# Performance work log

Measured on AMD Instinct MI355X. Metric: run time of the kernel, lower is better.

## Reference

```python
import jax, jax.numpy as jnp
import numpy as np

DEPTH = 4  # truncation depth of the signature


def setup_inputs() -> dict:
    key = jax.random.key(0)
    # (N, L, C) batch of paths
    path = jax.random.normal(key, (32, 256, 8), dtype=jnp.float32)
    return {"path": path}


def _signature(path, depth):
    """Truncated path signature via Chen's relation over linear segments.

    For a linear segment with increment dx, its signature is exp(dx) in the
    tensor algebra: level j = dx^{\otimes j} / j!.  The signature of the
    concatenated path is the tensor-algebra product of segment signatures,
    computed with a scan over segments.
    """
    N, L, C = path.shape
    dx = path[:, 1:, :] - path[:, :-1, :]  # (N, L-1, C) increments

    def exp_levels(d):
        # levels of exp(d): e_j = d^{\otimes j} / j!, flattened to (N, C^j)
        levels = [d]
        for j in range(2, depth + 1):
            nxt = jnp.einsum('na,nb->nab', levels[-1], d).reshape(N, -1) / j
            levels.append(nxt)
        return levels

    def step(carry, d):
        # carry: tuple of (N, C^k) for k = 1..depth (levels of running signature)
        # Chen: new_k = sum_{i+j=k} carry_i (x) e_j, with carry_0 = e_0 = 1
        e = exp_levels(d)
        new = []
        for k in range(1, depth + 1):
            acc = carry[k - 1] + e[k - 1]  # i=k,j=0 and i=0,j=k terms
            for i in range(1, k):
                acc = acc + jnp.einsum(
                    'na,nb->nab', carry[i - 1], e[k - i - 1]
                ).reshape(N, -1)
            new.append(acc)
        return tuple(new), None

    init = tuple(jnp.zeros((N, C ** k), path.dtype) for k in range(1, depth + 1))
    final, _ = jax.lax.scan(step, init, jnp.swapaxes(dx, 0, 1))  # scan over L-1
    return jnp.concatenate(final, axis=-1)  # (N, C + C^2 + ... + C^depth)


def reference(path):
    return _signature(path, DEPTH)
```

## Files before the change

kernel.cpp:

```cpp
#include <hip/hip_runtime.h>

#define NBATCH 32
#define LPATH 256
#define NSEG 255
#define SIGLEN 4680
#define INV6 (1.0f/6.0f)
#define INV24 (1.0f/24.0f)

struct __align__(16) CBuf {
    float T4t[64 * 64];
    float T3b[8 * 68];
    float T2[64];
    float T1[8];
};

__global__ __launch_bounds__(512) void sig_kernel(const float* __restrict__ path,
                                                  float* __restrict__ out) {
    const int n = blockIdx.x;
    const int t = threadIdx.x;
    const int w = t >> 6;
    const int l = t & 63;
    const int a = l >> 3;
    const int b = l & 7;

    __shared__ float dbuf[NSEG * 8];
    __shared__ CBuf bufs[4];

    const float* prow = path + n * (LPATH * 8);
    for (int i = t; i < NSEG * 8; i += 512) dbuf[i] = prow[i + 8] - prow[i];
    __syncthreads();

    float S4[64];
    float S3[8];
    #pragma unroll
    for (int j = 0; j < 64; ++j) S4[j] = 0.f;
    #pragma unroll
    for (int c = 0; c < 8; ++c) S3[c] = 0.f;
    float S2 = 0.f, a1a = 0.f;

    const int s0 = w * 32;
    const int s1 = (s0 + 32 < NSEG) ? (s0 + 32) : NSEG;
    for (int s = s0; s < s1; ++s) {
        const float4 dlo = *(const float4*)&dbuf[s * 8];
        const float4 dhi = *(const float4*)&dbuf[s * 8 + 4];
        const float dr[8] = {dlo.x, dlo.y, dlo.z, dlo.w, dhi.x, dhi.y, dhi.z, dhi.w};
        const float da = dbuf[s * 8 + a];
        const float db = dbuf[s * 8 + b];
        const float dab = da * db;
        const float P = dab * INV24 + a1a * db * INV6 + S2 * 0.5f;
        const float Q = dab * INV6  + a1a * db * 0.5f + S2;
        float K[8];
        #pragma unroll
        for (int c = 0; c < 8; ++c) K[c] = dr[c] * P + S3[c];
        #pragma unroll
        for (int c = 0; c < 8; ++c)
            #pragma unroll
            for (int e = 0; e < 8; ++e)
                S4[c * 8 + e] += dr[e] * K[c];
        #pragma unroll
        for (int c = 0; c < 8; ++c) S3[c] += dr[c] * Q;
        S2 += db * (da * 0.5f + a1a);
        a1a += da;
    }

    #pragma unroll
    for (int r = 0; r < 3; ++r) {
        const int stride = 1 << r;
        const int m = (stride << 1) - 1;

        if ((w & m) == stride) {
            CBuf& B = bufs[w >> (r + 1)];
            #pragma unroll
            for (int c = 0; c < 8; ++c)
                #pragma unroll
                for (int e = 0; e < 8; ++e)
                    B.T4t[(c * 8 + e) * 64 + l] = S4[c * 8 + e];
            #pragma unroll
            for (int c = 0; c < 8; ++c)
                B.T3b[a * 68 + b * 8 + c] = S3[c];
            B.T2[l] = S2;
            if (b == 0) B.T1[a] = a1a;
        }
        __syncthreads();

        if ((w & m) == 0) {
            const CBuf& B = bufs[w >> (r + 1)];
            const float4 t1lo = *(const float4*)&B.T1[0];
            const float4 t1hi = *(const float4*)&B.T1[4];
            const float t1r[8] = {t1lo.x, t1lo.y, t1lo.z, t1lo.w,
                                  t1hi.x, t1hi.y, t1hi.z, t1hi.w};
            const float t1a = B.T1[a];
            const float t1b = B.T1[b];
            #pragma unroll
            for (int c = 0; c < 8; ++c) {
                const float4 t2lo = *(const float4*)&B.T2[c * 8];
                const float4 t2hi = *(const float4*)&B.T2[c * 8 + 4];
                const float t2r[8] = {t2lo.x, t2lo.y, t2lo.z, t2lo.w,
                                      t2hi.x, t2hi.y, t2hi.z, t2hi.w};
                const float4 t3lo = *(const float4*)&B.T3b[b * 68 + c * 8];
                const float4 t3hi = *(const float4*)&B.T3b[b * 68 + c * 8 + 4];
                const float t3r[8] = {t3lo.x, t3lo.y, t3lo.z, t3lo.w,
                                      t3hi.x, t3hi.y, t3hi.z, t3hi.w};
                #pragma unroll
                for (int e = 0; e < 8; ++e)
                    S4[c * 8 + e] += S3[c] * t1r[e] + S2 * t2r[e]
                                   + a1a * t3r[e] + B.T4t[(c * 8 + e) * 64 + l];
            }
            #pragma unroll
            for (int c = 0; c < 8; ++c)
                S3[c] += S2 * t1r[c] + a1a * B.T2[b * 8 + c]
                       + B.T3b[a * 68 + b * 8 + c];
            S2 += a1a * t1b + B.T2[l];
            a1a += t1a;
        }
        __syncthreads();
    }

    if (w == 0) {
        float* o = out + n * SIGLEN;
        if (b == 0) o[a] = a1a;
        o[8 + l] = S2;
        *(float4*)&o[72 + l * 8]     = make_float4(S3[0], S3[1], S3[2], S3[3]);
        *(float4*)&o[72 + l * 8 + 4] = make_float4(S3[4], S3[5], S3[6], S3[7]);
        #pragma unroll
        for (int q = 0; q < 16; ++q)
            *(float4*)&o[584 + l * 64 + q * 4] =
                make_float4(S4[q * 4], S4[q * 4 + 1], S4[q * 4 + 2], S4[q * 4 + 3]);
    }
}

extern "C" void kernel_launch(void* const* d_in, const int* in_sizes, int n_in,
                              void* d_out, int out_size, void* d_ws, size_t ws_size,
                              hipStream_t stream) {
    const float* path = (const float*)d_in[0];
    float* out = (float*)d_out;
    sig_kernel<<<NBATCH, 512, 0, stream>>>(path, out);
}
```

Baseline: 20.82 us.

## Split signature scan into chunked kernel plus combine kernel across more blocks

The single 32-block kernel becomes two launches. First, 256 blocks each compute partial signatures for 32 segments (four per wave) and reduce them with a Chen tree into workspace. Second, a 32-block kernel merges the eight chunk signatures per path with the same tree. This spreads the serial per-wave scan over many more CUs, at the cost of a second launch and a round trip through global workspace.

Result: slower. 25.64 us (+23.2%).

```diff
diff --git a/kernel.cpp b/kernel.cpp
--- a/kernel.cpp
+++ b/kernel.cpp
@@ -4,6 +4,7 @@
 #define LPATH 256
 #define NSEG 255
 #define SIGLEN 4680
+#define PSTRIDE 4736
 #define INV6 (1.0f/6.0f)
 #define INV24 (1.0f/24.0f)
 
@@ -14,33 +15,93 @@
     float T1[8];
 };
 
-__global__ __launch_bounds__(512) void sig_kernel(const float* __restrict__ path,
-                                                  float* __restrict__ out) {
-    const int n = blockIdx.x;
+__device__ __forceinline__ void publish_sig(CBuf& B, const float S4[64],
+                                            const float S3[8], float S2, float a1a,
+                                            int l, int a, int b) {
+    #pragma unroll
+    for (int c = 0; c < 8; ++c)
+        #pragma unroll
+        for (int e = 0; e < 8; ++e)
+            B.T4t[(c * 8 + e) * 64 + l] = S4[c * 8 + e];
+    #pragma unroll
+    for (int c = 0; c < 8; ++c)
+        B.T3b[a * 68 + b * 8 + c] = S3[c];
+    B.T2[l] = S2;
+    if (b == 0) B.T1[a] = a1a;
+}
+
+__device__ __forceinline__ void absorb_sig(const CBuf& B, float S4[64], float S3[8],
+                                           float& S2, float& a1a, int l, int a, int b) {
+    const float4 t1lo = *(const float4*)&B.T1[0];
+    const float4 t1hi = *(const float4*)&B.T1[4];
+    const float t1r[8] = {t1lo.x, t1lo.y, t1lo.z, t1lo.w,
+                          t1hi.x, t1hi.y, t1hi.z, t1hi.w};
+    const float t1a = B.T1[a];
+    const float t1b = B.T1[b];
+    #pragma unroll
+    for (int c = 0; c < 8; ++c) {
+        const float4 t2lo = *(const float4*)&B.T2[c * 8];
+        const float4 t2hi = *(const float4*)&B.T2[c * 8 + 4];
+        const float t2r[8] = {t2lo.x, t2lo.y, t2lo.z, t2lo.w,
+                              t2hi.x, t2hi.y, t2hi.z, t2hi.w};
+        const float4 t3lo = *(const float4*)&B.T3b[b * 68 + c * 8];
+        const float4 t3hi = *(const float4*)&B.T3b[b * 68 + c * 8 + 4];
+        const float t3r[8] = {t3lo.x, t3lo.y, t3lo.z, t3lo.w,
+                              t3hi.x, t3hi.y, t3hi.z, t3hi.w};
+        #pragma unroll
+        for (int e = 0; e < 8; ++e)
+            S4[c * 8 + e] += S3[c] * t1r[e] + S2 * t2r[e]
+                           + a1a * t3r[e] + B.T4t[(c * 8 + e) * 64 + l];
+    }
+    #pragma unroll
+    for (int c = 0; c < 8; ++c)
+        S3[c] += S2 * t1r[c] + a1a * B.T2[b * 8 + c] + B.T3b[a * 68 + b * 8 + c];
+    S2 += a1a * t1b + B.T2[l];
+    a1a += t1a;
+}
+
+__device__ __forceinline__ void tree3(CBuf* bufs, float S4[64], float S3[8],
+                                      float& S2, float& a1a, int w, int l, int a, int b) {
+    #pragma unroll
+    for (int r = 0; r < 3; ++r) {
+        const int stride = 1 << r;
+        const int m = (stride << 1) - 1;
+        if ((w & m) == stride)
+            publish_sig(bufs[w >> (r + 1)], S4, S3, S2, a1a, l, a, b);
+        __syncthreads();
+        if ((w & m) == 0)
+            absorb_sig(bufs[w >> (r + 1)], S4, S3, S2, a1a, l, a, b);
+        __syncthreads();
+    }
+}
+
+__global__ __launch_bounds__(512) void sig_chunk_kernel(const float* __restrict__ path,
+                                                        float* __restrict__ ws) {
+    const int blk = blockIdx.x;
+    const int n  = blk >> 3;
+    const int cb = blk & 7;
     const int t = threadIdx.x;
-    const int w = t >> 6;
-    const int l = t & 63;
-    const int a = l >> 3;
-    const int b = l & 7;
+    const int w = t >> 6, l = t & 63, a = l >> 3, b = l & 7;
 
-    __shared__ float dbuf[NSEG * 8];
+    __shared__ float dbuf[32 * 8];
     __shared__ CBuf bufs[4];
 
-    const float* prow = path + n * (LPATH * 8);
-    for (int i = t; i < NSEG * 8; i += 512) dbuf[i] = prow[i + 8] - prow[i];
+    const float* prow = path + n * (LPATH * 8) + cb * 256;
+    for (int i = t; i < 32 * 8; i += 512) {
+        const int seg = cb * 32 + (i >> 3);
+        dbuf[i] = (seg < NSEG) ? (prow[i + 8] - prow[i]) : 0.f;
+    }
     __syncthreads();
 
-    float S4[64];
-    float S3[8];
+    float S4[64], S3[8], S2 = 0.f, a1a = 0.f;
     #pragma unroll
     for (int j = 0; j < 64; ++j) S4[j] = 0.f;
     #pragma unroll
     for (int c = 0; c < 8; ++c) S3[c] = 0.f;
-    float S2 = 0.f, a1a = 0.f;
 
-    const int s0 = w * 32;
-    const int s1 = (s0 + 32 < NSEG) ? (s0 + 32) : NSEG;
-    for (int s = s0; s < s1; ++s) {
+    #pragma unroll
+    for (int ss = 0; ss < 4; ++ss) {
+        const int s = w * 4 + ss;
         const float4 dlo = *(const float4*)&dbuf[s * 8];
         const float4 dhi = *(const float4*)&dbuf[s * 8 + 4];
         const float dr[8] = {dlo.x, dlo.y, dlo.z, dlo.w, dhi.x, dhi.y, dhi.z, dhi.w};
@@ -63,58 +124,46 @@
         a1a += da;
     }
 
+    tree3(bufs, S4, S3, S2, a1a, w, l, a, b);
+
+    if (w == 0) {
+        float* o = ws + blk * PSTRIDE;
+        if (b == 0) o[a] = a1a;
+        o[8 + l] = S2;
+        *(float4*)&o[72 + l * 8]     = make_float4(S3[0], S3[1], S3[2], S3[3]);
+        *(float4*)&o[72 + l * 8 + 4] = make_float4(S3[4], S3[5], S3[6], S3[7]);
+        #pragma unroll
+        for (int q = 0; q < 16; ++q)
+            *(float4*)&o[584 + l * 64 + q * 4] =
+                make_float4(S4[q * 4], S4[q * 4 + 1], S4[q * 4 + 2], S4[q * 4 + 3]);
+    }
+}
+
+__global__ __launch_bounds__(512) void sig_combine_kernel(const float* __restrict__ ws,
+                                                          float* __restrict__ out) {
+    const int n = blockIdx.x;
+    const int t = threadIdx.x;
+    const int w = t >> 6, l = t & 63, a = l >> 3, b = l & 7;
+
+    __shared__ CBuf bufs[4];
+
+    const float* p = ws + (n * 8 + w) * PSTRIDE;
+    float S4[64], S3[8], S2, a1a;
     #pragma unroll
-    for (int r = 0; r < 3; ++r) {
-        const int stride = 1 << r;
-        const int m = (stride << 1) - 1;
+    for (int q = 0; q < 16; ++q) {
+        const float4 v = *(const float4*)&p[584 + l * 64 + q * 4];
+        S4[q * 4] = v.x; S4[q * 4 + 1] = v.y; S4[q * 4 + 2] = v.z; S4[q * 4 + 3] = v.w;
+    }
+    {
+        const float4 v0 = *(const float4*)&p[72 + l * 8];
+        const float4 v1 = *(const float4*)&p[72 + l * 8 + 4];
+        S3[0] = v0.x; S3[1] = v0.y; S3[2] = v0.z; S3[3] = v0.w;
+        S3[4] = v1.x; S3[5] = v1.y; S3[6] = v1.z; S3[7] = v1.w;
+    }
+    S2 = p[8 + l];
+    a1a = p[a];
 
-        if ((w & m) == stride) {
-            CBuf& B = bufs[w >> (r + 1)];
-            #pragma unroll
-            for (int c = 0; c < 8; ++c)
-                #pragma unroll
-                for (int e = 0; e < 8; ++e)
-                    B.T4t[(c * 8 + e) * 64 + l] = S4[c * 8 + e];
-            #pragma unroll
-            for (int c = 0; c < 8; ++c)
-                B.T3b[a * 68 + b * 8 + c] = S3[c];
-            B.T2[l] = S2;
-            if (b == 0) B.T1[a] = a1a;
-        }
-        __syncthreads();
-
-        if ((w & m) == 0) {
-            const CBuf& B = bufs[w >> (r + 1)];
-            const float4 t1lo = *(const float4*)&B.T1[0];
-            const float4 t1hi = *(const float4*)&B.T1[4];
-            const float t1r[8] = {t1lo.x, t1lo.y, t1lo.z, t1lo.w,
-                                  t1hi.x, t1hi.y, t1hi.z, t1hi.w};
-            const float t1a = B.T1[a];
-            const float t1b = B.T1[b];
-            #pragma unroll
-            for (int c = 0; c < 8; ++c) {
-                const float4 t2lo = *(const float4*)&B.T2[c * 8];
-                const float4 t2hi = *(const float4*)&B.T2[c * 8 + 4];
-                const float t2r[8] = {t2lo.x, t2lo.y, t2lo.z, t2lo.w,
-                                      t2hi.x, t2hi.y, t2hi.z, t2hi.w};
-                const float4 t3lo = *(const float4*)&B.T3b[b * 68 + c * 8];
-                const float4 t3hi = *(const float4*)&B.T3b[b * 68 + c * 8 + 4];
-                const float t3r[8] = {t3lo.x, t3lo.y, t3lo.z, t3lo.w,
-                                      t3hi.x, t3hi.y, t3hi.z, t3hi.w};
-                #pragma unroll
-                for (int e = 0; e < 8; ++e)
-                    S4[c * 8 + e] += S3[c] * t1r[e] + S2 * t2r[e]
-                                   + a1a * t3r[e] + B.T4t[(c * 8 + e) * 64 + l];
-            }
-            #pragma unroll
-            for (int c = 0; c < 8; ++c)
-                S3[c] += S2 * t1r[c] + a1a * B.T2[b * 8 + c]
-                       + B.T3b[a * 68 + b * 8 + c];
-            S2 += a1a * t1b + B.T2[l];
-            a1a += t1a;
-        }
-        __syncthreads();
-    }
+    tree3(bufs, S4, S3, S2, a1a, w, l, a, b);
 
     if (w == 0) {
         float* o = out + n * SIGLEN;
@@ -133,6 +182,8 @@
                               void* d_out, int out_size, void* d_ws, size_t ws_size,
                               hipStream_t stream) {
     const float* path = (const float*)d_in[0];
+    float* ws = (float*)d_ws;
     float* out = (float*)d_out;
-    sig_kernel<<<NBATCH, 512, 0, stream>>>(path, out);
+    sig_chunk_kernel<<<NBATCH * 8, 512, 0, stream>>>(path, ws);
+    sig_combine_kernel<<<NBATCH, 512, 0, stream>>>(ws, out);
 }
```

## Use 16 waves per path with cooperative block-wide Chen tree merge

Applied to the files above, without the earlier changes.

Raises the block from 8 to 16 wavefronts, so each wave scans 16 segments instead of 32, and computes increments straight from global memory instead of staging them in shared memory. After one pairwise register merge, the remaining tree levels are done cooperatively, with all 1024 threads splitting the tensor-product work over shared-memory buffers, instead of only one wave doing each merge serially. This is meant to shorten the serial scan and the reduction critical path. In exchange it uses more shared memory and adds extra barriers and redundant global loads.

Result: slower. 49.07 us (+135.7%).

```diff
diff --git a/kernel.cpp b/kernel.cpp
--- a/kernel.cpp
+++ b/kernel.cpp
@@ -14,38 +14,79 @@
     float T1[8];
 };
 
-__global__ __launch_bounds__(512) void sig_kernel(const float* __restrict__ path,
-                                                  float* __restrict__ out) {
+__device__ __forceinline__ void publish_sig(CBuf& B, const float S4[64],
+                                            const float S3[8], float S2, float a1a,
+                                            int l, int a, int b) {
+    #pragma unroll
+    for (int c = 0; c < 8; ++c)
+        #pragma unroll
+        for (int e = 0; e < 8; ++e)
+            B.T4t[(c * 8 + e) * 64 + l] = S4[c * 8 + e];
+    #pragma unroll
+    for (int c = 0; c < 8; ++c)
+        B.T3b[a * 68 + b * 8 + c] = S3[c];
+    B.T2[l] = S2;
+    if (b == 0) B.T1[a] = a1a;
+}
+
+__device__ __forceinline__ void absorb_sig(const CBuf& B, float S4[64], float S3[8],
+                                           float& S2, float& a1a, int l, int a, int b) {
+    const float4 t1lo = *(const float4*)&B.T1[0];
+    const float4 t1hi = *(const float4*)&B.T1[4];
+    const float t1r[8] = {t1lo.x, t1lo.y, t1lo.z, t1lo.w,
+                          t1hi.x, t1hi.y, t1hi.z, t1hi.w};
+    const float t1a = B.T1[a];
+    const float t1b = B.T1[b];
+    #pragma unroll
+    for (int c = 0; c < 8; ++c) {
+        const float4 t2lo = *(const float4*)&B.T2[c * 8];
+        const float4 t2hi = *(const float4*)&B.T2[c * 8 + 4];
+        const float t2r[8] = {t2lo.x, t2lo.y, t2lo.z, t2lo.w,
+                              t2hi.x, t2hi.y, t2hi.z, t2hi.w};
+        const float4 t3lo = *(const float4*)&B.T3b[b * 68 + c * 8];
+        const float4 t3hi = *(const float4*)&B.T3b[b * 68 + c * 8 + 4];
+        const float t3r[8] = {t3lo.x, t3lo.y, t3lo.z, t3lo.w,
+                              t3hi.x, t3hi.y, t3hi.z, t3hi.w};
+        #pragma unroll
+        for (int e = 0; e < 8; ++e)
+            S4[c * 8 + e] += S3[c] * t1r[e] + S2 * t2r[e]
+                           + a1a * t3r[e] + B.T4t[(c * 8 + e) * 64 + l];
+    }
+    #pragma unroll
+    for (int c = 0; c < 8; ++c)
+        S3[c] += S2 * t1r[c] + a1a * B.T2[b * 8 + c] + B.T3b[a * 68 + b * 8 + c];
+    S2 += a1a * t1b + B.T2[l];
+    a1a += t1a;
+}
+
+__global__ __launch_bounds__(1024, 4) void sig_kernel(const float* __restrict__ path,
+                                                      float* __restrict__ out) {
     const int n = blockIdx.x;
     const int t = threadIdx.x;
-    const int w = t >> 6;
-    const int l = t & 63;
-    const int a = l >> 3;
-    const int b = l & 7;
-
-    __shared__ float dbuf[NSEG * 8];
-    __shared__ CBuf bufs[4];
+    const int w = t >> 6, l = t & 63, a = l >> 3, b = l & 7;
+
+    __shared__ CBuf bufs[8];
 
     const float* prow = path + n * (LPATH * 8);
-    for (int i = t; i < NSEG * 8; i += 512) dbuf[i] = prow[i + 8] - prow[i];
-    __syncthreads();
-
-    float S4[64];
-    float S3[8];
+
+    float S4[64], S3[8], S2 = 0.f, a1a = 0.f;
     #pragma unroll
     for (int j = 0; j < 64; ++j) S4[j] = 0.f;
     #pragma unroll
     for (int c = 0; c < 8; ++c) S3[c] = 0.f;
-    float S2 = 0.f, a1a = 0.f;
-
-    const int s0 = w * 32;
-    const int s1 = (s0 + 32 < NSEG) ? (s0 + 32) : NSEG;
-    for (int s = s0; s < s1; ++s) {
-        const float4 dlo = *(const float4*)&dbuf[s * 8];
-        const float4 dhi = *(const float4*)&dbuf[s * 8 + 4];
-        const float dr[8] = {dlo.x, dlo.y, dlo.z, dlo.w, dhi.x, dhi.y, dhi.z, dhi.w};
-        const float da = dbuf[s * 8 + a];
-        const float db = dbuf[s * 8 + b];
+
+    #pragma unroll
+    for (int ss = 0; ss < 16; ++ss) {
+        const int s = w * 16 + ss;
+        const int s1 = (s < NSEG) ? s + 1 : s;
+        const float4 alo = *(const float4*)&prow[s * 8];
+        const float4 ahi = *(const float4*)&prow[s * 8 + 4];
+        const float4 blo = *(const float4*)&prow[s1 * 8];
+        const float4 bhi = *(const float4*)&prow[s1 * 8 + 4];
+        const float dr[8] = {blo.x - alo.x, blo.y - alo.y, blo.z - alo.z, blo.w - alo.w,
+                             bhi.x - ahi.x, bhi.y - ahi.y, bhi.z - ahi.z, bhi.w - ahi.w};
+        const float da = prow[s1 * 8 + a] - prow[s * 8 + a];
+        const float db = prow[s1 * 8 + b] - prow[s * 8 + b];
         const float dab = da * db;
         const float P = dab * INV24 + a1a * db * INV6 + S2 * 0.5f;
         const float Q = dab * INV6  + a1a * db * 0.5f + S2;
@@ -63,69 +104,180 @@
         a1a += da;
     }
 
-    #pragma unroll
-    for (int r = 0; r < 3; ++r) {
-        const int stride = 1 << r;
-        const int m = (stride << 1) - 1;
-
-        if ((w & m) == stride) {
-            CBuf& B = bufs[w >> (r + 1)];
-            #pragma unroll
-            for (int c = 0; c < 8; ++c)
-                #pragma unroll
-                for (int e = 0; e < 8; ++e)
-                    B.T4t[(c * 8 + e) * 64 + l] = S4[c * 8 + e];
-            #pragma unroll
-            for (int c = 0; c < 8; ++c)
-                B.T3b[a * 68 + b * 8 + c] = S3[c];
-            B.T2[l] = S2;
-            if (b == 0) B.T1[a] = a1a;
-        }
-        __syncthreads();
-
-        if ((w & m) == 0) {
-            const CBuf& B = bufs[w >> (r + 1)];
-            const float4 t1lo = *(const float4*)&B.T1[0];
-            const float4 t1hi = *(const float4*)&B.T1[4];
-            const float t1r[8] = {t1lo.x, t1lo.y, t1lo.z, t1lo.w,
-                                  t1hi.x, t1hi.y, t1hi.z, t1hi.w};
-            const float t1a = B.T1[a];
-            const float t1b = B.T1[b];
-            #pragma unroll
-            for (int c = 0; c < 8; ++c) {
-                const float4 t2lo = *(const float4*)&B.T2[c * 8];
-                const float4 t2hi = *(const float4*)&B.T2[c * 8 + 4];
-                const float t2r[8] = {t2lo.x, t2lo.y, t2lo.z, t2lo.w,
-                                      t2hi.x, t2hi.y, t2hi.z, t2hi.w};
-                const float4 t3lo = *(const float4*)&B.T3b[b * 68 + c * 8];
-                const float4 t3hi = *(const float4*)&B.T3b[b * 68 + c * 8 + 4];
-                const float t3r[8] = {t3lo.x, t3lo.y, t3lo.z, t3lo.w,
-                                      t3hi.x, t3hi.y, t3hi.z, t3hi.w};
-                #pragma unroll
-                for (int e = 0; e < 8; ++e)
-                    S4[c * 8 + e] += S3[c] * t1r[e] + S2 * t2r[e]
-                                   + a1a * t3r[e] + B.T4t[(c * 8 + e) * 64 + l];
+    if (w & 1) publish_sig(bufs[w >> 1], S4, S3, S2, a1a, l, a, b);
+    __syncthreads();
+    if (!(w & 1)) absorb_sig(bufs[w >> 1], S4, S3, S2, a1a, l, a, b);
+    __syncthreads();
+
+    if (!(w & 1)) publish_sig(bufs[w >> 1], S4, S3, S2, a1a, l, a, b);
+    __syncthreads();
+
+    const int ce = t >> 4;
+    const int cc = ce >> 3, ee = ce & 7;
+    const int l0 = (t & 15) * 4;
+    const int aa = l0 >> 3, b0 = l0 & 7;
+
+    {
+        float r4[16];
+        #pragma unroll
+        for (int k = 0; k < 4; ++k) {
+            const CBuf& L = bufs[2 * k];
+            const CBuf& R = bufs[2 * k + 1];
+            const float4 A4 = *(const float4*)&L.T4t[ce * 64 + l0];
+            const float4 T4 = *(const float4*)&R.T4t[ce * 64 + l0];
+            const float4 A2 = *(const float4*)&L.T2[l0];
+            const float T1e = R.T1[ee];
+            const float T2ce = R.T2[cc * 8 + ee];
+            const float A1a = L.T1[aa];
+            const float A4r[4] = {A4.x, A4.y, A4.z, A4.w};
+            const float T4r[4] = {T4.x, T4.y, T4.z, T4.w};
+            const float A2r[4] = {A2.x, A2.y, A2.z, A2.w};
+            #pragma unroll
+            for (int j = 0; j < 4; ++j) {
+                const float A3s = L.T3b[aa * 68 + (b0 + j) * 8 + cc];
+                const float T3s = R.T3b[(b0 + j) * 68 + cc * 8 + ee];
+                r4[k * 4 + j] = A4r[j] + A3s * T1e + A2r[j] * T2ce + A1a * T3s + T4r[j];
             }
-            #pragma unroll
-            for (int c = 0; c < 8; ++c)
-                S3[c] += S2 * t1r[c] + a1a * B.T2[b * 8 + c]
-                       + B.T3b[a * 68 + b * 8 + c];
-            S2 += a1a * t1b + B.T2[l];
-            a1a += t1a;
-        }
-        __syncthreads();
-    }
-
-    if (w == 0) {
+        }
+        float r3[2];
+        #pragma unroll
+        for (int jj = 0; jj < 2; ++jj) {
+            const int f = 2 * t + jj;
+            const int p = f >> 9, idx = f & 511;
+            const CBuf& L = bufs[2 * p];
+            const CBuf& R = bufs[2 * p + 1];
+            const int a3 = idx >> 6, b3 = (idx >> 3) & 7, c3 = idx & 7;
+            r3[jj] = L.T3b[a3 * 68 + b3 * 8 + c3] + L.T2[a3 * 8 + b3] * R.T1[c3]
+                   + L.T1[a3] * R.T2[b3 * 8 + c3] + R.T3b[a3 * 68 + b3 * 8 + c3];
+        }
+        float r2 = 0.f, r1 = 0.f;
+        if (t < 256) {
+            const int p = t >> 6, idx = t & 63;
+            r2 = bufs[2 * p].T2[idx] + bufs[2 * p].T1[idx >> 3] * bufs[2 * p + 1].T1[idx & 7]
+               + bufs[2 * p + 1].T2[idx];
+        }
+        if (t < 32) r1 = bufs[2 * (t >> 3)].T1[t & 7] + bufs[2 * (t >> 3) + 1].T1[t & 7];
+        __syncthreads();
+        #pragma unroll
+        for (int k = 0; k < 4; ++k)
+            *(float4*)&bufs[2 * k].T4t[ce * 64 + l0] =
+                make_float4(r4[k * 4], r4[k * 4 + 1], r4[k * 4 + 2], r4[k * 4 + 3]);
+        #pragma unroll
+        for (int jj = 0; jj < 2; ++jj) {
+            const int f = 2 * t + jj;
+            const int p = f >> 9, idx = f & 511;
+            bufs[2 * p].T3b[(idx >> 6) * 68 + ((idx >> 3) & 7) * 8 + (idx & 7)] = r3[jj];
+        }
+        if (t < 256) bufs[2 * (t >> 6)].T2[t & 63] = r2;
+        if (t < 32)  bufs[2 * (t >> 3)].T1[t & 7] = r1;
+        __syncthreads();
+    }
+
+    {
+        float r4[8];
+        #pragma unroll
+        for (int k = 0; k < 2; ++k) {
+            const CBuf& L = bufs[4 * k];
+            const CBuf& R = bufs[4 * k + 2];
+            const float4 A4 = *(const float4*)&L.T4t[ce * 64 + l0];
+            const float4 T4 = *(const float4*)&R.T4t[ce * 64 + l0];
+            const float4 A2 = *(const float4*)&L.T2[l0];
+            const float T1e = R.T1[ee];
+            const float T2ce = R.T2[cc * 8 + ee];
+            const float A1a = L.T1[aa];
+            const float A4r[4] = {A4.x, A4.y, A4.z, A4.w};
+            const float T4r[4] = {T4.x, T4.y, T4.z, T4.w};
+            const float A2r[4] = {A2.x, A2.y, A2.z, A2.w};
+            #pragma unroll
+            for (int j = 0; j < 4; ++j) {
+                const float A3s = L.T3b[aa * 68 + (b0 + j) * 8 + cc];
+                const float T3s = R.T3b[(b0 + j) * 68 + cc * 8 + ee];
+                r4[k * 4 + j] = A4r[j] + A3s * T1e + A2r[j] * T2ce + A1a * T3s + T4r[j];
+            }
+        }
+        float r3;
+        {
+            const int p = t >> 9, idx = t & 511;
+            const CBuf& L = bufs[4 * p];
+            const CBuf& R = bufs[4 * p + 2];
+            const int a3 = idx >> 6, b3 = (idx >> 3) & 7, c3 = idx & 7;
+            r3 = L.T3b[a3 * 68 + b3 * 8 + c3] + L.T2[a3 * 8 + b3] * R.T1[c3]
+               + L.T1[a3] * R.T2[b3 * 8 + c3] + R.T3b[a3 * 68 + b3 * 8 + c3];
+        }
+        float r2 = 0.f, r1 = 0.f;
+        if (t < 128) {
+            const int p = t >> 6, idx = t & 63;
+            r2 = bufs[4 * p].T2[idx] + bufs[4 * p].T1[idx >> 3] * bufs[4 * p + 2].T1[idx & 7]
+               + bufs[4 * p + 2].T2[idx];
+        }
+        if (t < 16) r1 = bufs[4 * (t >> 3)].T1[t & 7] + bufs[4 * (t >> 3) + 2].T1[t & 7];
+        __syncthreads();
+        #pragma unroll
+        for (int k = 0; k < 2; ++k)
+            *(float4*)&bufs[4 * k].T4t[ce * 64 + l0] =
+                make_float4(r4[k * 4], r4[k * 4 + 1], r4[k * 4 + 2], r4[k * 4 + 3]);
+        {
+            const int p = t >> 9, idx = t & 511;
+            bufs[4 * p].T3b[(idx >> 6) * 68 + ((idx >> 3) & 7) * 8 + (idx & 7)] = r3;
+        }
+        if (t < 128) bufs[4 * (t >> 6)].T2[t & 63] = r2;
+        if (t < 16)  bufs[4 * (t >> 3)].T1[t & 7] = r1;
+        __syncthreads();
+    }
+
+    {
+        const CBuf& L = bufs[0];
+        const CBuf& R = bufs[4];
         float* o = out + n * SIGLEN;
-        if (b == 0) o[a] = a1a;
-        o[8 + l] = S2;
-        *(float4*)&o[72 + l * 8]     = make_float4(S3[0], S3[1], S3[2], S3[3]);
-        *(float4*)&o[72 + l * 8 + 4] = make_float4(S3[4], S3[5], S3[6], S3[7]);
-        #pragma unroll
-        for (int q = 0; q < 16; ++q)
-            *(float4*)&o[584 + l * 64 + q * 4] =
-                make_float4(S4[q * 4], S4[q * 4 + 1], S4[q * 4 + 2], S4[q * 4 + 3]);
+        {
+            const int abc = t >> 1, e0 = (t & 1) * 4;
+            const int a4 = abc >> 6, b4 = (abc >> 3) & 7, c4 = abc & 7;
+            const int ll = a4 * 8 + b4;
+            const float4 T1v = *(const float4*)&R.T1[e0];
+            const float4 T2v = *(const float4*)&R.T2[c4 * 8 + e0];
+            const float4 T3v = *(const float4*)&R.T3b[b4 * 68 + c4 * 8 + e0];
+            const float A3s = L.T3b[a4 * 68 + b4 * 8 + c4];
+            const float A2s = L.T2[ll];
+            const float A1s = L.T1[a4];
+            const float T1r[4] = {T1v.x, T1v.y, T1v.z, T1v.w};
+            const float T2r[4] = {T2v.x, T2v.y, T2v.z, T2v.w};
+            const float T3r[4] = {T3v.x, T3v.y, T3v.z, T3v.w};
+            float rv[4];
+            #pragma unroll
+            for (int j = 0; j < 4; ++j)
+                rv[j] = L.T4t[(c4 * 8 + e0 + j) * 64 + ll]
+                      + A3s * T1r[j] + A2s * T2r[j] + A1s * T3r[j]
+                      + R.T4t[(c4 * 8 + e0 + j) * 64 + ll];
+            *(float4*)&o[584 + abc * 8 + e0] = make_float4(rv[0], rv[1], rv[2], rv[3]);
+        }
+        if (t < 128) {
+            const int ab = t >> 1, c0 = (t & 1) * 4;
+            const int a3 = ab >> 3, b3 = ab & 7;
+            float rv[4];
+            #pragma unroll
+            for (int j = 0; j < 4; ++j)
+                rv[j] = L.T3b[a3 * 68 + b3 * 8 + c0 + j]
+                      + L.T2[ab] * R.T1[c0 + j]
+                      + L.T1[a3] * R.T2[b3 * 8 + c0 + j]
+                      + R.T3b[a3 * 68 + b3 * 8 + c0 + j];
+            *(float4*)&o[72 + ab * 8 + c0] = make_float4(rv[0], rv[1], rv[2], rv[3]);
+        }
+        if (t < 16) {
+            const int a2 = t >> 1, b02 = (t & 1) * 4;
+            float rv[4];
+            #pragma unroll
+            for (int j = 0; j < 4; ++j)
+                rv[j] = L.T2[a2 * 8 + b02 + j] + L.T1[a2] * R.T1[b02 + j]
+                      + R.T2[a2 * 8 + b02 + j];
+            *(float4*)&o[8 + a2 * 8 + b02] = make_float4(rv[0], rv[1], rv[2], rv[3]);
+        }
+        if (t < 2) {
+            float rv[4];
+            #pragma unroll
+            for (int j = 0; j < 4; ++j)
+                rv[j] = L.T1[t * 4 + j] + R.T1[t * 4 + j];
+            *(float4*)&o[t * 4] = make_float4(rv[0], rv[1], rv[2], rv[3]);
+        }
     }
 }
 
@@ -134,5 +286,5 @@
                               hipStream_t stream) {
     const float* path = (const float*)d_in[0];
     float* out = (float*)d_out;
-    sig_kernel<<<NBATCH, 512, 0, stream>>>(path, out);
-}
+    sig_kernel<<<NBATCH, 1024, 0, stream>>>(path, out);
+}
```
